# Kernel optimization log

Hardware: AMD Instinct MI355X
Metric: run time of the kernel (lower is better)

## Reference

```python
import jax, jax.numpy as jnp
import numpy as np

B, P, C, H, W = 256, 512, 512, 7, 8
T = H * W  # 56
EPS = 1e-8


def setup_inputs() -> dict:
    key = jax.random.key(0)
    k1, k2, k3 = jax.random.split(key, 3)
    inp = jax.random.normal(k1, (B, C, H, W), dtype=jnp.float32)
    # xavier-uniform-like init for prototype (fan over last two dims as torch does)
    bound_p = float(np.sqrt(6.0 / (P + C * T)))
    prototype = jax.random.uniform(k2, (P, C, T), dtype=jnp.float32, minval=-bound_p, maxval=bound_p)
    bound_w = float(np.sqrt(6.0 / (C + 1)))
    fc_w = jax.random.uniform(k3, (1, C), dtype=jnp.float32, minval=-bound_w, maxval=bound_w)
    fc_b = jnp.zeros((1,), dtype=jnp.float32)
    return {"input": inp, "prototype": prototype, "fc_w": fc_w, "fc_b": fc_b}


def reference(input, prototype, fc_w, fc_b):
    # flatten spatial dims: (B, C, T)
    x = input.reshape(input.shape[0], input.shape[1], -1)
    # per-position cosine similarity over channel dim
    dots = jnp.einsum('bct,pct->bpt', x, prototype)          # (B, P, T)
    xn = jnp.linalg.norm(x, axis=1)                           # (B, T)
    pn = jnp.linalg.norm(prototype, axis=1)                   # (P, T)
    sim = dots / jnp.maximum(xn[:, None, :] * pn[None, :, :], EPS)
    att = jax.nn.softmax(sim, axis=-1)                        # (B, P, T)
    # attention-pooled elementwise product: (B, P, C)
    feat = jnp.einsum('bpt,bct,pct->bpc', att, x, prototype)
    # fc: Linear(C, 1) then relu, view to (B, P)
    out = jax.nn.relu(jnp.einsum('bpc,oc->bpo', feat, fc_w) + fc_b)
    return out.reshape(out.shape[0], out.shape[1])
```

## Files before the change

### kernel.cpp

```cpp
#include <hip/hip_runtime.h>
#include <hip/hip_bf16.h>
#include <math.h>

constexpr int kB = 256, kC = 512, kT = 56, kP = 512;
constexpr int kCT = kC * kT;

typedef short v4s __attribute__((ext_vector_type(4)));
typedef short v8s __attribute__((ext_vector_type(8)));
typedef float v4f __attribute__((ext_vector_type(4)));
typedef float v16f __attribute__((ext_vector_type(16)));

__device__ __forceinline__ unsigned pack_bf16(float a, float b) {
  __hip_bfloat16 ha = __float2bfloat16(a);
  __hip_bfloat16 hb = __float2bfloat16(b);
  unsigned short ua, ub;
  __builtin_memcpy(&ua, &ha, 2);
  __builtin_memcpy(&ub, &hb, 2);
  return (unsigned)ua | ((unsigned)ub << 16);
}

__device__ __forceinline__ v4s frag2(unsigned w0, unsigned w1) {
  unsigned u[2] = {w0, w1};
  v4s s;
  __builtin_memcpy(&s, u, 8);
  return s;
}

__device__ __forceinline__ v8s frag8(uint4 u) {
  v8s s;
  __builtin_memcpy(&s, &u, 16);
  return s;
}

#define GLOAD(gp, lp)                                                        \
  __builtin_amdgcn_global_load_lds(                                          \
      (const __attribute__((address_space(1))) unsigned*)(const unsigned*)(gp), \
      (__attribute__((address_space(3))) unsigned*)(unsigned*)(lp), 16, 0, 0)

__global__ __launch_bounds__(512) void prep_kernel(
    const float* __restrict__ x, const float* __restrict__ proto,
    const float* __restrict__ fcw,
    unsigned* __restrict__ xt, unsigned* __restrict__ xwt,
    unsigned* __restrict__ pt,
    float* __restrict__ xn, float* __restrict__ pn) {
  __shared__ float tile[128 * 57];
  __shared__ float fws[512];
  __shared__ float part[8][64];

  const int tid = threadIdx.x;
  const int n = blockIdx.x;
  const bool isx = (n < kB);
  const int row = isx ? n : (n - kB);
  const float* src = (isx ? x : proto) + (size_t)row * kCT;

  fws[tid] = fcw[tid & 511];

  const int g = tid >> 6, tt = tid & 63;
  float nacc = 0.f;

#pragma unroll 1
  for (int ch = 0; ch < 4; ++ch) {
    const float* csrc = src + ch * (128 * 56);
#pragma unroll
    for (int it = 0; it < 4; ++it) {
      const int idx = it * 512 + tid;
      if (idx < 1792) {
        const int f0 = idx * 4;
        float4 v = *(const float4*)(csrc + f0);
        int c = (int)(((unsigned)f0 * 74899u) >> 22);
        int t = f0 - c * 56;
        tile[c * 57 + t] = v.x;
        tile[c * 57 + t + 1] = v.y;
        tile[c * 57 + t + 2] = v.z;
        tile[c * 57 + t + 3] = v.w;
      }
    }
    __syncthreads();
    if (tt < 56) {
#pragma unroll
      for (int cc2 = 0; cc2 < 16; ++cc2) {
        float u = tile[(g * 16 + cc2) * 57 + tt];
        nacc = fmaf(u, u, nacc);
      }
    }
#pragma unroll
    for (int it = 0; it < 7; ++it) {
      const int id = it * 512 + tid;
      const int t = id >> 6;
      const int cw = id & 63;
      float g0 = tile[(2 * cw) * 57 + t];
      float g1 = tile[(2 * cw + 1) * 57 + t];
      unsigned wd = pack_bf16(g0, g1);
      if (isx) {
        const size_t o = ((size_t)(t * kB + row)) * 256 + ch * 64 + cw;
        const int c = ch * 128 + 2 * cw;
        xt[o] = wd;
        xwt[o] = pack_bf16(g0 * fws[c], g1 * fws[c + 1]);
      } else {
        pt[((size_t)(t * kP + row)) * 256 + ch * 64 + cw] = wd;
      }
    }
    __syncthreads();
  }

  part[g][tt] = nacc;
  __syncthreads();
  if (tid < 56) {
    float s = 0.f;
#pragma unroll
    for (int gg = 0; gg < 8; ++gg) s += part[gg][tid];
    float r = sqrtf(s);
    if (isx) xn[row * 56 + tid] = r; else pn[row * 56 + tid] = r;
  }
}

constexpr int TILE = 64 * 32;
constexpr int BUF = 3 * TILE;

__global__ __launch_bounds__(256, 2) void proto_gemm_kernel(
    const unsigned* __restrict__ xt, const unsigned* __restrict__ xwt,
    const unsigned* __restrict__ pt,
    const float* __restrict__ xn, const float* __restrict__ pn,
    float* __restrict__ part) {
  __shared__ __align__(16) unsigned lds[3 * BUF];
  __shared__ float xnL[4 * 64], pnL[4 * 64];

  const int tid = threadIdx.x;
  const int l = tid & 63;
  const int w4 = tid >> 6;
  const int wm = w4 >> 1;
  const int wn = w4 & 1;

  int bid = (int)blockIdx.x;
  bid = (bid & 7) * 56 + (bid >> 3);
  const int b0 = (bid & 3) * 64;
  const int p0 = ((bid >> 2) & 7) * 64;
  const int tg = bid >> 5;

  {
    const int tl = tid >> 6, r = tid & 63;
    xnL[tid] = xn[(b0 + r) * 56 + tg * 4 + tl];
    pnL[tid] = pn[(p0 + r) * 56 + tg * 4 + tl];
  }
  __syncthreads();

  const int lrow = l >> 3, lch = l & 7;
  size_t xsrc[2], psrc[2];
  int ldst[2];
#pragma unroll
  for (int j = 0; j < 2; ++j) {
    const int row = w4 * 16 + j * 8 + lrow;
    const int ch4 = ((lch ^ (row & 7))) * 4;
    xsrc[j] = (size_t)(b0 + row) * 256 + ch4;
    psrc[j] = (size_t)(p0 + row) * 256 + ch4;
    ldst[j] = (w4 * 16 + j * 8) * 32;
  }

  const int fr = l & 31;
  const int hi = l >> 5;
  const int axb = (wm * 32 + fr) * 32;
  const int pxb = (wn * 32 + fr) * 32;
  const int frs = fr & 7;

  v16f aD, aW, sac, nac;
#pragma unroll
  for (int i = 0; i < 16; ++i) { aD[i] = 0.f; aW[i] = 0.f; sac[i] = 0.f; nac[i] = 0.f; }

  auto STAGE = [&](int s, int buf) {
    const int t = tg * 4 + (s >> 3);
    const size_t xo = (size_t)t * (kB * 256) + (size_t)((s & 7) * 32);
    const size_t po = (size_t)t * (kP * 256) + (size_t)((s & 7) * 32);
    unsigned* lb = lds + buf * BUF;
#pragma unroll
    for (int j = 0; j < 2; ++j) {
      GLOAD(xt + xsrc[j] + xo, lb + ldst[j]);
      GLOAD(xwt + xsrc[j] + xo, lb + TILE + ldst[j]);
      GLOAD(pt + psrc[j] + po, lb + 2 * TILE + ldst[j]);
    }
  };

  auto COMPUTE = [&](int s, int buf) {
    const unsigned* bx = lds + buf * BUF;
#pragma unroll
    for (int ks = 0; ks < 4; ++ks) {
      const int col = (((ks << 1) | hi) ^ frs) << 2;
      v8s xf = frag8(*(const uint4*)(bx + axb + col));
      v8s wf = frag8(*(const uint4*)(bx + TILE + axb + col));
      v8s pf = frag8(*(const uint4*)(bx + 2 * TILE + pxb + col));
      aD = __builtin_amdgcn_mfma_f32_32x32x16_bf16(xf, pf, aD, 0, 0, 0);
      aW = __builtin_amdgcn_mfma_f32_32x32x16_bf16(wf, pf, aW, 0, 0, 0);
    }
    if ((s & 7) == 7) {
      const int tl = s >> 3;
      const float pnv = pnL[tl * 64 + wn * 32 + fr];
#pragma unroll
      for (int i = 0; i < 16; ++i) {
        const int drow = (i & 3) + 8 * (i >> 2) + 4 * hi;
        float xnv = pnv;
        xnv = xnL[tl * 64 + wm * 32 + drow];
        float den = fmaxf(xnv * pnv, 1e-8f);
        float sim = aD[i] * __builtin_amdgcn_rcpf(den);
        float e = __expf(sim);
        sac[i] += e;
        nac[i] = fmaf(e, aW[i], nac[i]);
        aD[i] = 0.f;
        aW[i] = 0.f;
      }
    }
  };

  STAGE(0, 0);
  STAGE(1, 1);

  int c0 = 0, c1 = 1, c2 = 2;
#pragma unroll 1
  for (int s = 0; s < 32; ++s) {
    if (s < 31) asm volatile("s_waitcnt vmcnt(6)" ::: "memory");
    else        asm volatile("s_waitcnt vmcnt(0)" ::: "memory");
    __builtin_amdgcn_s_barrier();
    __builtin_amdgcn_sched_barrier(0);
    COMPUTE(s, c0);
    if (s < 30) STAGE(s + 2, c2);
    const int tmp = c0; c0 = c1; c1 = c2; c2 = tmp;
  }

  float* psb = part + ((size_t)tg * 2 + 0) * 131072;
  float* pnb = part + ((size_t)tg * 2 + 1) * 131072;
#pragma unroll
  for (int i = 0; i < 16; ++i) {
    const int drow = (i & 3) + 8 * (i >> 2) + 4 * hi;
    const size_t o = (size_t)(b0 + wm * 32 + drow) * 512 + p0 + wn * 32 + fr;
    psb[o] = sac[i];
    pnb[o] = nac[i];
  }
}

__global__ __launch_bounds__(256) void merge_kernel(
    const float* __restrict__ part, const float* __restrict__ fcb,
    float* __restrict__ out) {
  const int pair = blockIdx.x * 256 + threadIdx.x;
  float S = 0.f, N = 0.f;
#pragma unroll
  for (int k = 0; k < 14; ++k) {
    S += part[((size_t)k * 2 + 0) * 131072 + pair];
    N += part[((size_t)k * 2 + 1) * 131072 + pair];
  }
  float o = N * __builtin_amdgcn_rcpf(S) + fcb[0];
  out[pair] = fmaxf(o, 0.f);
}

__global__ __launch_bounds__(1024) void proto_mfma_kernel(
    const float* __restrict__ x, const float* __restrict__ proto,
    const float* __restrict__ fcw, const float* __restrict__ fcb,
    float* __restrict__ out) {
  __shared__ unsigned xs[56 * 289];
  __shared__ unsigned ps[56 * 145];
  __shared__ unsigned pws[56 * 145];

  const int tid = threadIdx.x;
  const int l = tid & 63;
  const int w = tid >> 6;
  const int bq = w & 1;
  const int tq = w >> 1;
  const int t0 = tq * 7;

  const int n = blockIdx.y * 32 + blockIdx.x;
  const int p0 = (n >> 3) * 16;
  const int b0 = (n & 7) * 32;

  const bool act = (l < 56);
  const int lt = l;

  const int xbase0 = ((b0 + 2 * w + 0) * kC) * kT + lt;
  const int xbase1 = ((b0 + 2 * w + 1) * kC) * kT + lt;
  const int pbase = ((p0 + w) * kC) * kT + lt;

  const int arow = l & 15;
  const int q2 = (l >> 4) << 1;
  const int xoff = (bq * 16 + arow) * 9 + q2;
  const int poff = arow * 9 + q2;

  v4f acc[7][2];
#pragma unroll
  for (int ti = 0; ti < 7; ++ti) {
    acc[ti][0] = v4f{0.f, 0.f, 0.f, 0.f};
    acc[ti][1] = v4f{0.f, 0.f, 0.f, 0.f};
  }
  float xn2a = 0.f, xn2b = 0.f, pn2 = 0.f;

#pragma unroll 1
  for (int st = 0; st < 32; ++st) {
    const int k0 = st * 16;
    if (act) {
#pragma unroll
      for (int r = 0; r < 16; ++r) {
        const int cw = r & 7;
        const int c = k0 + 2 * cw;
        const int ga = ((r >> 3) ? xbase1 : xbase0) + c * kT;
        float g0 = x[ga], g1 = x[ga + kT];
        if (r >> 3) xn2b = fmaf(g0, g0, fmaf(g1, g1, xn2b));
        else xn2a = fmaf(g0, g0, fmaf(g1, g1, xn2a));
        xs[lt * 289 + (2 * w + (r >> 3)) * 9 + cw] = pack_bf16(g0, g1);
      }
#pragma unroll
      for (int cw = 0; cw < 8; ++cw) {
        const int c = k0 + 2 * cw;
        const int ga = pbase + c * kT;
        float g0 = proto[ga], g1 = proto[ga + kT];
        pn2 = fmaf(g0, g0, fmaf(g1, g1, pn2));
        ps[lt * 145 + w * 9 + cw] = pack_bf16(g0, g1);
        float f0 = fcw[c], f1 = fcw[c + 1];
        pws[lt * 145 + w * 9 + cw] = pack_bf16(g0 * f0, g1 * f1);
      }
    }
    __syncthreads();
#pragma unroll
    for (int ti = 0; ti < 7; ++ti) {
      const int t = t0 + ti;
      unsigned xw0 = xs[t * 289 + xoff];
      unsigned xw1 = xs[t * 289 + xoff + 1];
      unsigned pw0 = ps[t * 145 + poff];
      unsigned pw1 = ps[t * 145 + poff + 1];
      unsigned ww0 = pws[t * 145 + poff];
      unsigned ww1 = pws[t * 145 + poff + 1];
      v4s af = frag2(xw0, xw1);
      v4s bf = frag2(pw0, pw1);
      v4s wf = frag2(ww0, ww1);
      acc[ti][0] = __builtin_amdgcn_mfma_f32_16x16x16bf16_1k(af, bf, acc[ti][0], 0, 0, 0);
      acc[ti][1] = __builtin_amdgcn_mfma_f32_16x16x16bf16_1k(af, wf, acc[ti][1], 0, 0, 0);
    }
    __syncthreads();
  }

  float* xnorm = (float*)ps;
  float* pnorm = xnorm + 32 * 56;
  if (act) {
    xnorm[(2 * w + 0) * 56 + lt] = xn2a;
    xnorm[(2 * w + 1) * 56 + lt] = xn2b;
    pnorm[w * 56 + lt] = pn2;
  }
  __syncthreads();

  float* fm = (float*)xs;
  float* fsum = fm + 4096;
  float* fnum = fsum + 4096;
  const int pc = arow;
  const int qq = l >> 4;
#pragma unroll
  for (int i = 0; i < 4; ++i) {
    const int bl = bq * 16 + 4 * qq + i;
    float m = -3.0e38f;
    float sims[7];
#pragma unroll
    for (int ti = 0; ti < 7; ++ti) {
      const int t = t0 + ti;
      float den = fmaxf(sqrtf(xnorm[bl * 56 + t]) * sqrtf(pnorm[pc * 56 + t]), 1e-8f);
      float s = acc[ti][0][i] / den;
      sims[ti] = s;
      m = fmaxf(m, s);
    }
    float se = 0.f, nu = 0.f;
#pragma unroll
    for (int ti = 0; ti < 7; ++ti) {
      float e = __expf(sims[ti] - m);
      se += e;
      nu = fmaf(e, acc[ti][1][i], nu);
    }
    const int pair = bl * 16 + pc;
    fm[tq * 512 + pair] = m;
    fsum[tq * 512 + pair] = se;
    fnum[tq * 512 + pair] = nu;
  }
  __syncthreads();

  if (tid < 512) {
    float M = -3.0e38f;
#pragma unroll
    for (int k = 0; k < 8; ++k) M = fmaxf(M, fm[k * 512 + tid]);
    float S = 0.f, N = 0.f;
#pragma unroll
    for (int k = 0; k < 8; ++k) {
      float sc = __expf(fm[k * 512 + tid] - M);
      S = fmaf(fsum[k * 512 + tid], sc, S);
      N = fmaf(fnum[k * 512 + tid], sc, N);
    }
    float o = N / S + fcb[0];
    out[(b0 + (tid >> 4)) * kP + p0 + (tid & 15)] = fmaxf(o, 0.f);
  }
}

extern "C" void kernel_launch(void* const* d_in, const int* in_sizes, int n_in,
                              void* d_out, int out_size, void* d_ws, size_t ws_size,
                              hipStream_t stream) {
  const float* x = (const float*)d_in[0];
  const float* proto = (const float*)d_in[1];
  const float* fcw = (const float*)d_in[2];
  const float* fcb = (const float*)d_in[3];
  float* out = (float*)d_out;

  const size_t need = 73572352;
  if (ws_size >= need) {
    unsigned* xt = (unsigned*)d_ws;
    unsigned* xwt = xt + 3670016;
    unsigned* ptb = xt + 7340032;
    float* partb = (float*)(xt + 14680064);
    float* xnb = (float*)(xt + 18350080);
    float* pnb = xnb + 14336;

    hipLaunchKernelGGL(prep_kernel, dim3(kB + kP), dim3(512), 0, stream,
                       x, proto, fcw, xt, xwt, ptb, xnb, pnb);
    hipLaunchKernelGGL(proto_gemm_kernel, dim3(448), dim3(256), 0, stream,
                       xt, xwt, ptb, xnb, pnb, partb);
    hipLaunchKernelGGL(merge_kernel, dim3(512), dim3(256), 0, stream,
                       partb, fcb, out);
  } else {
    hipLaunchKernelGGL(proto_mfma_kernel, dim3(32, 8), dim3(1024), 0, stream,
                       x, proto, fcw, fcb, out);
  }
}
```

Baseline: 61.58 us.

## Split prep kernel across channel chunks with atomic norm accumulation

```diff
diff --git a/kernel.cpp b/kernel.cpp
--- a/kernel.cpp
+++ b/kernel.cpp
@@ -42,13 +42,15 @@
     const float* __restrict__ fcw,
     unsigned* __restrict__ xt, unsigned* __restrict__ xwt,
     unsigned* __restrict__ pt,
-    float* __restrict__ xn, float* __restrict__ pn) {
+    float* __restrict__ xn2, float* __restrict__ pn2) {
   __shared__ float tile[128 * 57];
   __shared__ float fws[512];
   __shared__ float part[8][64];
 
   const int tid = threadIdx.x;
-  const int n = blockIdx.x;
+  const int bidx = blockIdx.x;
+  const int n = bidx >> 2;
+  const int ch = bidx & 3;
   const bool isx = (n < kB);
   const int row = isx ? n : (n - kB);
   const float* src = (isx ? x : proto) + (size_t)row * kCT;
@@ -56,51 +58,49 @@
   fws[tid] = fcw[tid & 511];
 
   const int g = tid >> 6, tt = tid & 63;
+
+  const float* csrc = src + ch * (128 * 56);
+#pragma unroll
+  for (int it = 0; it < 4; ++it) {
+    const int idx = it * 512 + tid;
+    if (idx < 1792) {
+      const int f0 = idx * 4;
+      float4 v = *(const float4*)(csrc + f0);
+      int c = (int)(((unsigned)f0 * 74899u) >> 22);
+      int t = f0 - c * 56;
+      tile[c * 57 + t] = v.x;
+      tile[c * 57 + t + 1] = v.y;
+      tile[c * 57 + t + 2] = v.z;
+      tile[c * 57 + t + 3] = v.w;
+    }
+  }
+  __syncthreads();
+
   float nacc = 0.f;
-
-#pragma unroll 1
-  for (int ch = 0; ch < 4; ++ch) {
-    const float* csrc = src + ch * (128 * 56);
-#pragma unroll
-    for (int it = 0; it < 4; ++it) {
-      const int idx = it * 512 + tid;
-      if (idx < 1792) {
-        const int f0 = idx * 4;
-        float4 v = *(const float4*)(csrc + f0);
-        int c = (int)(((unsigned)f0 * 74899u) >> 22);
-        int t = f0 - c * 56;
-        tile[c * 57 + t] = v.x;
-        tile[c * 57 + t + 1] = v.y;
-        tile[c * 57 + t + 2] = v.z;
-        tile[c * 57 + t + 3] = v.w;
-      }
-    }
-    __syncthreads();
-    if (tt < 56) {
-#pragma unroll
-      for (int cc2 = 0; cc2 < 16; ++cc2) {
-        float u = tile[(g * 16 + cc2) * 57 + tt];
-        nacc = fmaf(u, u, nacc);
-      }
-    }
-#pragma unroll
-    for (int it = 0; it < 7; ++it) {
-      const int id = it * 512 + tid;
-      const int t = id >> 6;
-      const int cw = id & 63;
-      float g0 = tile[(2 * cw) * 57 + t];
-      float g1 = tile[(2 * cw + 1) * 57 + t];
-      unsigned wd = pack_bf16(g0, g1);
-      if (isx) {
-        const size_t o = ((size_t)(t * kB + row)) * 256 + ch * 64 + cw;
-        const int c = ch * 128 + 2 * cw;
-        xt[o] = wd;
-        xwt[o] = pack_bf16(g0 * fws[c], g1 * fws[c + 1]);
-      } else {
-        pt[((size_t)(t * kP + row)) * 256 + ch * 64 + cw] = wd;
-      }
-    }
-    __syncthreads();
+  if (tt < 56) {
+#pragma unroll
+    for (int cc2 = 0; cc2 < 16; ++cc2) {
+      float u = tile[(g * 16 + cc2) * 57 + tt];
+      nacc = fmaf(u, u, nacc);
+    }
+  }
+
+#pragma unroll
+  for (int it = 0; it < 7; ++it) {
+    const int id = it * 512 + tid;
+    const int t = id >> 6;
+    const int cw = id & 63;
+    float g0 = tile[(2 * cw) * 57 + t];
+    float g1 = tile[(2 * cw + 1) * 57 + t];
+    unsigned wd = pack_bf16(g0, g1);
+    if (isx) {
+      const size_t o = ((size_t)(t * kB + row)) * 256 + ch * 64 + cw;
+      const int c = ch * 128 + 2 * cw;
+      xt[o] = wd;
+      xwt[o] = pack_bf16(g0 * fws[c], g1 * fws[c + 1]);
+    } else {
+      pt[((size_t)(t * kP + row)) * 256 + ch * 64 + cw] = wd;
+    }
   }
 
   part[g][tt] = nacc;
@@ -109,8 +109,8 @@
     float s = 0.f;
 #pragma unroll
     for (int gg = 0; gg < 8; ++gg) s += part[gg][tid];
-    float r = sqrtf(s);
-    if (isx) xn[row * 56 + tid] = r; else pn[row * 56 + tid] = r;
+    if (isx) atomicAdd(&xn2[row * 56 + tid], s);
+    else     atomicAdd(&pn2[row * 56 + tid], s);
   }
 }
 
@@ -120,7 +120,7 @@
 __global__ __launch_bounds__(256, 2) void proto_gemm_kernel(
     const unsigned* __restrict__ xt, const unsigned* __restrict__ xwt,
     const unsigned* __restrict__ pt,
-    const float* __restrict__ xn, const float* __restrict__ pn,
+    const float* __restrict__ xn2, const float* __restrict__ pn2,
     float* __restrict__ part) {
   __shared__ __align__(16) unsigned lds[3 * BUF];
   __shared__ float xnL[4 * 64], pnL[4 * 64];
@@ -139,8 +139,8 @@
 
   {
     const int tl = tid >> 6, r = tid & 63;
-    xnL[tid] = xn[(b0 + r) * 56 + tg * 4 + tl];
-    pnL[tid] = pn[(p0 + r) * 56 + tg * 4 + tl];
+    xnL[tid] = sqrtf(xn2[(b0 + r) * 56 + tg * 4 + tl]);
+    pnL[tid] = sqrtf(pn2[(p0 + r) * 56 + tg * 4 + tl]);
   }
   __syncthreads();
 
@@ -196,8 +196,7 @@
 #pragma unroll
       for (int i = 0; i < 16; ++i) {
         const int drow = (i & 3) + 8 * (i >> 2) + 4 * hi;
-        float xnv = pnv;
-        xnv = xnL[tl * 64 + wm * 32 + drow];
+        const float xnv = xnL[tl * 64 + wm * 32 + drow];
         float den = fmaxf(xnv * pnv, 1e-8f);
         float sim = aD[i] * __builtin_amdgcn_rcpf(den);
         float e = __expf(sim);
@@ -404,13 +403,15 @@
     unsigned* xwt = xt + 3670016;
     unsigned* ptb = xt + 7340032;
     float* partb = (float*)(xt + 14680064);
-    float* xnb = (float*)(xt + 18350080);
-    float* pnb = xnb + 14336;
-
-    hipLaunchKernelGGL(prep_kernel, dim3(kB + kP), dim3(512), 0, stream,
-                       x, proto, fcw, xt, xwt, ptb, xnb, pnb);
+    float* xn2b = (float*)(xt + 18350080);
+    float* pn2b = xn2b + 14336;
+
+    hipMemsetAsync(xn2b, 0, (14336 + 28672) * sizeof(float), stream);
+
+    hipLaunchKernelGGL(prep_kernel, dim3(4 * (kB + kP)), dim3(512), 0, stream,
+                       x, proto, fcw, xt, xwt, ptb, xn2b, pn2b);
     hipLaunchKernelGGL(proto_gemm_kernel, dim3(448), dim3(256), 0, stream,
-                       xt, xwt, ptb, xnb, pnb, partb);
+                       xt, xwt, ptb, xn2b, pn2b, partb);
     hipLaunchKernelGGL(merge_kernel, dim3(512), dim3(256), 0, stream,
                        partb, fcb, out);
   } else {
```

Measured after the change: 67.05 us. 8.9% more time.
